# Performance work log

Hardware: AMD Instinct MI355X
Metric: run time of the kernel (lower is better)

The kernel has to match this reference:

```python
import jax, jax.numpy as jnp
import numpy as np

D_MODEL = 2048
D_STATE = 64
D_CONV = 4
EXPAND = 2
HEADDIM = 64
NGROUPS = 1
CHUNK = 64
D_INNER = EXPAND * D_MODEL            # 4096
NHEADS = D_INNER // HEADDIM           # 64
D_XBC = D_INNER + 2 * NGROUPS * D_STATE
D_IN_PROJ = 2 * D_INNER + 2 * NGROUPS * D_STATE + NHEADS


def setup_inputs():
    key = jax.random.key(0)
    ks = jax.random.split(key, 8)
    B, L = 2, 4096
    u = jax.random.normal(ks[0], (B, L, D_MODEL), jnp.float32)
    W_in = jax.random.normal(ks[1], (D_IN_PROJ, D_MODEL), jnp.float32) * 0.02
    conv_w = jax.random.normal(ks[2], (D_XBC, D_CONV), jnp.float32) * 0.2
    conv_b = jnp.zeros((D_XBC,), jnp.float32)
    dt = jnp.exp(jax.random.uniform(ks[3], (NHEADS,)) * (np.log(0.1) - np.log(0.001)) + np.log(0.001))
    dt = jnp.clip(dt, 1e-4)
    dt_bias = dt + jnp.log(-jnp.expm1(-dt))
    A_log = jnp.log(jax.random.uniform(ks[4], (NHEADS,), minval=1.0, maxval=16.0))
    D_param = jnp.ones((NHEADS,), jnp.float32)
    norm_w = jnp.ones((D_INNER,), jnp.float32)
    W_out = jax.random.normal(ks[5], (D_MODEL, D_INNER), jnp.float32) * 0.02
    return dict(u=u, W_in=W_in, conv_w=conv_w, conv_b=conv_b, dt_bias=dt_bias,
                A_log=A_log, D_param=D_param, norm_w=norm_w, W_out=W_out)


def segsum(x):
    # x: (..., T) -> (..., T, T) with entry [l,s] = sum_{s< i <= l} x[i], -inf above diag
    T = x.shape[-1]
    mask_strict = jnp.tril(jnp.ones((T, T), bool), k=-1)
    mask_incl = jnp.tril(jnp.ones((T, T), bool), k=0)
    xe = jnp.where(mask_strict, x[..., :, None], 0.0)  # element [l,s] = x[l] if l>s
    xseg = jnp.cumsum(xe, axis=-2)
    return jnp.where(mask_incl, xseg, -jnp.inf)


def ssd_scan(X, A, Bm, Cm, block_len=CHUNK):
    # X: (b,L,h,p), A: (b,L,h), Bm/Cm: (b,L,h,n)
    b, seqlen, h, p = X.shape
    n = Bm.shape[-1]
    pad_len = (block_len - seqlen % block_len) % block_len
    if pad_len > 0:
        X = jnp.pad(X, ((0, 0), (0, pad_len), (0, 0), (0, 0)))
        A = jnp.pad(A, ((0, 0), (0, pad_len), (0, 0)))
        Bm = jnp.pad(Bm, ((0, 0), (0, pad_len), (0, 0), (0, 0)))
        Cm = jnp.pad(Cm, ((0, 0), (0, pad_len), (0, 0), (0, 0)))
    L = X.shape[1]
    c = L // block_len
    Xc = X.reshape(b, c, block_len, h, p)
    Ac = A.reshape(b, c, block_len, h).transpose(0, 3, 1, 2)  # (b,h,c,l)
    Bc = Bm.reshape(b, c, block_len, h, n)
    Cc = Cm.reshape(b, c, block_len, h, n)
    A_cum = jnp.cumsum(Ac, axis=-1)                           # (b,h,c,l)
    Lmat = jnp.exp(segsum(Ac))                                # (b,h,c,l,s)
    CB = jnp.einsum('bclhn,bcshn->bhcls', Cc, Bc)
    Y_diag = jnp.einsum('bhcls,bcshp->bhclp', CB * Lmat, Xc)
    decay_states = jnp.exp(A_cum[..., -1:] - A_cum)           # (b,h,c,l)
    states = jnp.einsum('bhcl,bclhn,bclhp->bhcpn', decay_states, Bc, Xc)
    init = jnp.zeros((b, h, 1, p, n), X.dtype)
    states = jnp.concatenate([init, states], axis=2)          # (b,h,c+1,p,n)
    chunk_decay = jnp.pad(A_cum[..., -1], ((0, 0), (0, 0), (1, 0)))  # (b,h,c+1)
    decay_chunk = jnp.exp(segsum(chunk_decay))                # (b,h,c+1,c+1)
    new_states = jnp.einsum('bhzc,bhcpn->bhzpn', decay_chunk, states)[:, :, :-1]
    Y_off = jnp.einsum('bclhn,bhcpn,bhcl->bhclp', Cc, new_states, jnp.exp(A_cum))
    Y = (Y_diag + Y_off).transpose(0, 2, 3, 1, 4).reshape(b, L, h, p)
    if pad_len > 0:
        Y = Y[:, :seqlen]
    return Y


def rmsnorm_grouped(x, w, ngroups, eps=1e-5):
    gs = x.shape[-1] // ngroups
    xg = x.reshape(*x.shape[:-1], ngroups, gs)
    xg = xg * jax.lax.rsqrt(jnp.mean(xg * xg, axis=-1, keepdims=True) + eps)
    return xg.reshape(x.shape) * w


def reference(u, W_in, conv_w, conv_b, dt_bias, A_log, D_param, norm_w, W_out):
    B, L, _ = u.shape
    zxbcdt = u @ W_in.T                                      # (B,L,d_in_proj)
    z = zxbcdt[..., :D_INNER]
    xBC = zxbcdt[..., D_INNER:D_INNER + D_XBC]
    dt = zxbcdt[..., D_INNER + D_XBC:]
    # causal depthwise conv1d, kernel D_CONV, left-pad D_CONV-1
    xpad = jnp.pad(xBC, ((0, 0), (D_CONV - 1, 0), (0, 0)))
    conv = conv_b
    for k in range(D_CONV):
        conv = conv + conv_w[:, k] * xpad[:, k:k + L, :]
    xBC = jax.nn.silu(conv)
    x = xBC[..., :D_INNER].reshape(B, L, NHEADS, HEADDIM)
    B_ssm = xBC[..., D_INNER:D_INNER + NGROUPS * D_STATE].reshape(B, L, NGROUPS, D_STATE)
    C_ssm = xBC[..., D_INNER + NGROUPS * D_STATE:].reshape(B, L, NGROUPS, D_STATE)
    if NGROUPS < NHEADS:
        rep = NHEADS // NGROUPS
        B_ssm = jnp.repeat(B_ssm, rep, axis=2)
        C_ssm = jnp.repeat(C_ssm, rep, axis=2)
    dt = jax.nn.softplus(dt + dt_bias)                        # (B,L,nheads)
    A = -jnp.exp(A_log)                                       # (nheads,)
    y = ssd_scan(x * dt[..., None], A * dt, B_ssm, C_ssm, block_len=CHUNK)
    y = y + D_param[:, None] * x
    y = y.reshape(B, L, D_INNER)
    y = rmsnorm_grouped(y * jax.nn.silu(z), norm_w, NGROUPS)
    return y @ W_out.T
```

## Files before the change

kernel.cpp:

```cpp
#include <hip/hip_runtime.h>
#include <hip/hip_bf16.h>
#include <math.h>

#define SEQ       4096
#define DMODEL    2048
#define DINNER    4096
#define DXBC      4224
#define NPROJ     8384
#define NHEADS    64
#define HDIM      64
#define DSTATE    64
#define NCHUNK    64
#define XLD       4352

typedef __attribute__((ext_vector_type(8))) _Float16 half8;
typedef __attribute__((ext_vector_type(2))) _Float16 half2v;
typedef __attribute__((ext_vector_type(4))) float floatx4;

__device__ __forceinline__ void async_copy16(void* lds, const void* g) {
  __builtin_amdgcn_global_load_lds(
      (const __attribute__((address_space(1))) unsigned int*)g,
      (__attribute__((address_space(3))) unsigned int*)lds, 16, 0, 0);
}

__device__ __forceinline__ float silu_f(float x) { return x / (1.f + __expf(-x)); }

__device__ __forceinline__ void cvt8(const float* __restrict__ s, _Float16* __restrict__ d) {
  float4 a = *(const float4*)s;
  float4 b = *(const float4*)(s + 4);
  half8 h;
  h[0] = (_Float16)a.x; h[1] = (_Float16)a.y; h[2] = (_Float16)a.z; h[3] = (_Float16)a.w;
  h[4] = (_Float16)b.x; h[5] = (_Float16)b.y; h[6] = (_Float16)b.z; h[7] = (_Float16)b.w;
  *(half8*)d = h;
}

__global__ void diag_kernel(float* out, float v) { out[0] = v; }

#define U_N8 (SEQ * DMODEL / 8)
__global__ void cvt_in_kernel(const float* __restrict__ u, const float* __restrict__ W_in,
                              _Float16* __restrict__ ubf, _Float16* __restrict__ winbf) {
  int i = blockIdx.x * 256 + threadIdx.x;
  if (i < U_N8) {
    cvt8(u + (size_t)i * 8, ubf + (size_t)i * 8);
  } else {
    int j = i - U_N8;
    int row = j >> 8;
    size_t off = (size_t)j * 8;
    if (row < NPROJ) {
      cvt8(W_in + off, winbf + off);
    } else {
      half8 zz = {};
      *(half8*)(winbf + off) = zz;
    }
  }
}

__global__ void cvt8_kernel(const float* __restrict__ src, _Float16* __restrict__ dst, int n8) {
  int i = blockIdx.x * 256 + threadIdx.x;
  if (i < n8) cvt8(src + (size_t)i * 8, dst + (size_t)i * 8);
}

template <typename OT>
__global__ __launch_bounds__(256) void gemm_bt64(
    const _Float16* __restrict__ A, const _Float16* __restrict__ B,
    OT* __restrict__ C0, OT* __restrict__ C1, int K,
    int ldc0, int ldc1, int ncol0, int tiles_m, int tiles_n) {
  __shared__ __align__(16) _Float16 As[128 * 64];
  __shared__ __align__(16) _Float16 Bs[128 * 64];
  int t = threadIdx.x;
  int nt = tiles_m * tiles_n;
  int id = blockIdx.x;
  int id2 = ((nt & 7) == 0) ? ((id & 7) * (nt >> 3) + (id >> 3)) : id;
  int wband = tiles_m << 2;
  int g = id2 / wband;
  int rm = id2 - g * wband;
  int bw = tiles_n - (g << 2); if (bw > 4) bw = 4;
  int pn = (g << 2) + rm % bw;
  int pm = rm / bw;
  int m0 = pm * 128, n0 = pn * 128;

  int w = t >> 6, lane = t & 63, q = lane >> 4, r = lane & 15;
  int wm = (w >> 1) * 64, wn = (w & 1) * 64;
  int rowoff = lane >> 3;
  int chunkoff = ((lane & 7) ^ rowoff) * 8;
  const _Float16* gA[4];
  const _Float16* gB[4];
#pragma unroll
  for (int i = 0; i < 4; ++i) {
    gA[i] = A + (size_t)(m0 + i * 32 + w * 8 + rowoff) * K + chunkoff;
    gB[i] = B + (size_t)(n0 + i * 32 + w * 8 + rowoff) * K + chunkoff;
  }
  floatx4 acc[4][4] = {};
  for (int k0 = 0; k0 < K; k0 += 64) {
#pragma unroll
    for (int i = 0; i < 4; ++i) {
      async_copy16(As + (i * 32 + w * 8) * 64, gA[i] + k0);
      async_copy16(Bs + (i * 32 + w * 8) * 64, gB[i] + k0);
    }
    __syncthreads();
#pragma unroll
    for (int kk = 0; kk < 64; kk += 32) {
      half8 af[4], bf[4];
#pragma unroll
      for (int im = 0; im < 4; ++im) {
        int R = wm + im * 16 + r;
        af[im] = *(const half8*)&As[R * 64 + ((((kk >> 3) + q) ^ (R & 7)) << 3)];
      }
#pragma unroll
      for (int in = 0; in < 4; ++in) {
        int R = wn + in * 16 + r;
        bf[in] = *(const half8*)&Bs[R * 64 + ((((kk >> 3) + q) ^ (R & 7)) << 3)];
      }
#pragma unroll
      for (int im = 0; im < 4; ++im)
#pragma unroll
        for (int in = 0; in < 4; ++in)
          acc[im][in] =
              __builtin_amdgcn_mfma_f32_16x16x32_f16(af[im], bf[in], acc[im][in], 0, 0, 0);
    }
    __syncthreads();
  }
  OT* Cp = (n0 < ncol0) ? C0 : C1;
  int ldc = (n0 < ncol0) ? ldc0 : ldc1;
  int cb = (n0 < ncol0) ? n0 : n0 - ncol0;
#pragma unroll
  for (int im = 0; im < 4; ++im)
#pragma unroll
    for (int in = 0; in < 4; ++in)
#pragma unroll
      for (int i = 0; i < 4; ++i)
        Cp[(size_t)(m0 + wm + im * 16 + q * 4 + i) * ldc + cb + wn + in * 16 + r] =
            (OT)acc[im][in][i];
}

__global__ void conv_silu_kernel(const _Float16* __restrict__ xin, const float* __restrict__ conv_w,
                                 const float* __restrict__ conv_b, _Float16* __restrict__ xcv) {
  int idx = blockIdx.x * 256 + threadIdx.x;
  int l = idx / (DXBC / 2);
  int c = (idx - l * (DXBC / 2)) * 2;
  const _Float16* zc = xin + (size_t)l * XLD + c;
  float a0 = conv_b[c], a1 = conv_b[c + 1];
#pragma unroll
  for (int k = 0; k < 4; ++k) {
    int off = k - 3;
    if (l + off >= 0) {
      half2v v = *(const half2v*)(zc + (long)off * XLD);
      a0 += conv_w[c * 4 + k] * (float)v[0];
      a1 += conv_w[c * 4 + 4 + k] * (float)v[1];
    }
  }
  half2v o;
  o[0] = (_Float16)silu_f(a0);
  o[1] = (_Float16)silu_f(a1);
  *(half2v*)(xcv + (size_t)l * DXBC + c) = o;
}

__global__ __launch_bounds__(256) void dtscan_kernel(
    const _Float16* __restrict__ dtraw, const float* __restrict__ dt_bias,
    const float* __restrict__ A_log, float* __restrict__ dtp,
    float* __restrict__ acum, float* __restrict__ chs) {
  int c = blockIdx.x;
  __shared__ float dAs[64 * 65];
  int t = threadIdx.x;
  int h = t & 63;
  float bias = dt_bias[h];
  float negA = -__expf(A_log[h]);
#pragma unroll
  for (int i = 0; i < 16; ++i) {
    int l = i * 4 + (t >> 6);
    int row = c * 64 + l;
    float x = (float)dtraw[(size_t)row * XLD + h] + bias;
    float dtv = (x > 20.f) ? x : log1pf(__expf(x));
    dtp[(size_t)row * 64 + h] = dtv;
    dAs[l * 65 + h] = negA * dtv;
  }
  __syncthreads();
  if (t < 64) {
    float a = 0.f;
    size_t base = ((size_t)c * 64 + t) * 64;
    for (int l = 0; l < 64; ++l) {
      a += dAs[l * 65 + t];
      acum[base + l] = a;
    }
    chs[c * 64 + t] = a;
  }
}

__global__ __launch_bounds__(256) void states_kernel(
    const _Float16* __restrict__ xcv, const float* __restrict__ dtp,
    const float* __restrict__ acum, const float* __restrict__ chs,
    _Float16* __restrict__ states) {
  int bid = blockIdx.x;
  int c = bid & 63, h = bid >> 6;
  int row0 = c * 64;
  int acbase = (c * 64 + h) * 64;
  __shared__ __align__(16) _Float16 XdT[64 * 72];
  __shared__ __align__(16) _Float16 BdT[64 * 72];
  __shared__ float dec[64];
  int t = threadIdx.x;
  if (t < 64) dec[t] = __expf(chs[acbase >> 6] - acum[acbase + t]);
  __syncthreads();
#pragma unroll
  for (int i = 0; i < 16; ++i) {
    int flat = i * 256 + t;
    int l = flat >> 6, col = flat & 63;
    int grow = row0 + l;
    float dtv = dtp[(size_t)grow * 64 + h];
    float xv = (float)xcv[(size_t)grow * DXBC + h * 64 + col] * dtv;
    XdT[col * 72 + l] = (_Float16)xv;
    float bv = (float)xcv[(size_t)grow * DXBC + DINNER + col] * dec[l];
    BdT[col * 72 + l] = (_Float16)bv;
  }
  __syncthreads();
  int w = t >> 6, lane = t & 63, q = lane >> 4, r = lane & 15;
#pragma unroll
  for (int in = 0; in < 4; ++in) {
    floatx4 a4 = {0.f, 0.f, 0.f, 0.f};
#pragma unroll
    for (int k0 = 0; k0 < 64; k0 += 32) {
      half8 af = *(const half8*)&XdT[(w * 16 + r) * 72 + k0 + q * 8];
      half8 bf = *(const half8*)&BdT[(in * 16 + r) * 72 + k0 + q * 8];
      a4 = __builtin_amdgcn_mfma_f32_16x16x32_f16(af, bf, a4, 0, 0, 0);
    }
#pragma unroll
    for (int i = 0; i < 4; ++i)
      states[((size_t)bid * 64 + (w * 16 + q * 4 + i)) * 64 + in * 16 + r] = (_Float16)a4[i];
  }
}

__global__ __launch_bounds__(256) void scan_kernel(_Float16* __restrict__ states,
                                                   const float* __restrict__ chs) {
  int bid = blockIdx.x;
  int h = bid >> 4, seg = bid & 15;
  int e = seg * 256 + threadIdx.x;
  float carry = 0.f;
#pragma unroll 2
  for (int c = 0; c < 64; ++c) {
    size_t idx = ((size_t)(h * 64 + c)) * 4096 + e;
    float s = (float)states[idx];
    states[idx] = (_Float16)carry;
    carry = carry * __expf(chs[c * 64 + h]) + s;
  }
}

__global__ __launch_bounds__(256) void yout_kernel(
    const _Float16* __restrict__ xcv, const float* __restrict__ dtp,
    const float* __restrict__ acum, const _Float16* __restrict__ sin_,
    const float* __restrict__ Dp, _Float16* __restrict__ Y) {
  int bid = blockIdx.x;
  int c = bid & 63, h = bid >> 6;
  int row0 = c * 64;
  int acbase = (c * 64 + h) * 64;
  __shared__ __align__(16) _Float16 Cs[64 * 72];
  __shared__ __align__(16) _Float16 Bt[64 * 72];
  __shared__ __align__(16) _Float16 XdT[64 * 72];
  __shared__ __align__(16) _Float16 Ms[64 * 72];
  __shared__ float acs[64];
  int t = threadIdx.x;
  if (t < 64) acs[t] = acum[acbase + t];
#pragma unroll
  for (int i = 0; i < 16; ++i) {
    int flat = i * 256 + t;
    int l = flat >> 6, col = flat & 63;
    int grow = row0 + l;
    const _Float16* rp = xcv + (size_t)grow * DXBC;
    Cs[l * 72 + col] = rp[DINNER + DSTATE + col];
    Bt[l * 72 + col] = rp[DINNER + col];
    float xv = (float)rp[h * 64 + col] * dtp[(size_t)grow * 64 + h];
    XdT[col * 72 + l] = (_Float16)xv;
  }
  __syncthreads();
  int w = t >> 6, lane = t & 63, q = lane >> 4, r = lane & 15;
  int m = w * 16 + r;
#pragma unroll
  for (int in = 0; in < 4; ++in) {
    floatx4 cb = {0.f, 0.f, 0.f, 0.f};
#pragma unroll
    for (int k0 = 0; k0 < 64; k0 += 32) {
      half8 af = *(const half8*)&Cs[m * 72 + k0 + q * 8];
      half8 bf = *(const half8*)&Bt[(in * 16 + r) * 72 + k0 + q * 8];
      cb = __builtin_amdgcn_mfma_f32_16x16x32_f16(af, bf, cb, 0, 0, 0);
    }
#pragma unroll
    for (int i = 0; i < 4; ++i) {
      int l = w * 16 + q * 4 + i;
      int s = in * 16 + r;
      float v = (s <= l) ? cb[i] * __expf(acs[l] - acs[s]) : 0.f;
      Ms[l * 72 + s] = (_Float16)v;
    }
  }
  __syncthreads();
  size_t sbase = (size_t)bid * 4096;
  float Dh = Dp[h];
#pragma unroll
  for (int in = 0; in < 4; ++in) {
    floatx4 acc = {0.f, 0.f, 0.f, 0.f};
#pragma unroll
    for (int k0 = 0; k0 < 64; k0 += 32) {
      half8 af = *(const half8*)&Cs[m * 72 + k0 + q * 8];
      half8 bf = *(const half8*)&sin_[sbase + (size_t)(in * 16 + r) * 64 + k0 + q * 8];
      acc = __builtin_amdgcn_mfma_f32_16x16x32_f16(af, bf, acc, 0, 0, 0);
    }
#pragma unroll
    for (int i = 0; i < 4; ++i) acc[i] *= __expf(acs[w * 16 + q * 4 + i]);
#pragma unroll
    for (int k0 = 0; k0 < 64; k0 += 32) {
      half8 af = *(const half8*)&Ms[m * 72 + k0 + q * 8];
      half8 bf = *(const half8*)&XdT[(in * 16 + r) * 72 + k0 + q * 8];
      acc = __builtin_amdgcn_mfma_f32_16x16x32_f16(af, bf, acc, 0, 0, 0);
    }
#pragma unroll
    for (int i = 0; i < 4; ++i) {
      int l = w * 16 + q * 4 + i;
      int p = in * 16 + r;
      int grow = row0 + l;
      float xv = (float)xcv[(size_t)grow * DXBC + h * 64 + p];
      Y[(size_t)grow * DINNER + h * 64 + p] = (_Float16)(acc[i] + Dh * xv);
    }
  }
}

__global__ __launch_bounds__(256) void rmsnorm_kernel(const _Float16* __restrict__ Y,
                                                      _Float16* __restrict__ Z,
                                                      const float* __restrict__ norm_w) {
  int row = blockIdx.x;
  const half8* y8 = (const half8*)(Y + (size_t)row * DINNER);
  half8* z8 = (half8*)(Z + (size_t)row * DINNER);
  __shared__ float red[4];
  int t = threadIdx.x;
  float g[16];
  float ss = 0.f;
#pragma unroll
  for (int i = 0; i < 2; ++i) {
    int j = i * 256 + t;
    half8 yv = y8[j];
    half8 zv = z8[j];
#pragma unroll
    for (int e = 0; e < 8; ++e) {
      float gv = (float)yv[e] * silu_f((float)zv[e]);
      g[i * 8 + e] = gv;
      ss += gv * gv;
    }
  }
#pragma unroll
  for (int o = 32; o > 0; o >>= 1) ss += __shfl_down(ss, o, 64);
  if ((t & 63) == 0) red[t >> 6] = ss;
  __syncthreads();
  float rs = rsqrtf((red[0] + red[1] + red[2] + red[3]) / (float)DINNER + 1e-5f);
#pragma unroll
  for (int i = 0; i < 2; ++i) {
    int j = i * 256 + t;
    const float4* w4 = (const float4*)(norm_w + j * 8);
    float4 wa = w4[0], wb = w4[1];
    half8 o;
    o[0] = (_Float16)(g[i * 8 + 0] * rs * wa.x);
    o[1] = (_Float16)(g[i * 8 + 1] * rs * wa.y);
    o[2] = (_Float16)(g[i * 8 + 2] * rs * wa.z);
    o[3] = (_Float16)(g[i * 8 + 3] * rs * wa.w);
    o[4] = (_Float16)(g[i * 8 + 4] * rs * wb.x);
    o[5] = (_Float16)(g[i * 8 + 5] * rs * wb.y);
    o[6] = (_Float16)(g[i * 8 + 6] * rs * wb.z);
    o[7] = (_Float16)(g[i * 8 + 7] * rs * wb.w);
    z8[j] = o;
  }
}

extern "C" void kernel_launch(void* const* d_in, const int* in_sizes, int n_in,
                              void* d_out, int out_size, void* d_ws, size_t ws_size,
                              hipStream_t stream) {
  const float* u       = (const float*)d_in[0];
  const float* W_in    = (const float*)d_in[1];
  const float* conv_w  = (const float*)d_in[2];
  const float* conv_b  = (const float*)d_in[3];
  const float* dt_bias = (const float*)d_in[4];
  const float* A_log   = (const float*)d_in[5];
  const float* D_param = (const float*)d_in[6];
  const float* norm_w  = (const float*)d_in[7];
  const float* W_out   = (const float*)d_in[8];
  float* out = (float*)d_out;
  char* ws = (char*)d_ws;

  const size_t off_z      = 0;
  const size_t off_xbcdt  = 33554432ULL;
  const size_t off_Y      = 33554432ULL;
  const size_t off_xcv    = 69206016ULL;
  const size_t off_winbf  = 69206016ULL;
  const size_t off_states = 103809024ULL;
  const size_t off_ubf    = 103809024ULL;
  const size_t off_wout   = 103809024ULL;
  const size_t off_dtp    = 137363456ULL;
  const size_t off_acum   = 139460608ULL;
  const size_t off_chs    = 140509184ULL;
  const size_t ws_needed  = 140525568ULL;
  if (ws_size < ws_needed) {
    diag_kernel<<<1, 1, 0, stream>>>(out, (float)ws_size);
    return;
  }

  _Float16* zb     = (_Float16*)(ws + off_z);
  _Float16* xbcdtb = (_Float16*)(ws + off_xbcdt);
  _Float16* Yb     = (_Float16*)(ws + off_Y);
  _Float16* xcv    = (_Float16*)(ws + off_xcv);
  _Float16* winbf  = (_Float16*)(ws + off_winbf);
  _Float16* states = (_Float16*)(ws + off_states);
  _Float16* ubf    = (_Float16*)(ws + off_ubf);
  _Float16* woutbf = (_Float16*)(ws + off_wout);
  float*    dtp    = (float*)(ws + off_dtp);
  float*    acum   = (float*)(ws + off_acum);
  float*    chs    = (float*)(ws + off_chs);

  for (int b = 0; b < 2; ++b) {
    const float* ub = u + (size_t)b * SEQ * DMODEL;
    float* outb = out + (size_t)b * SEQ * DMODEL;

    cvt_in_kernel<<<U_N8 / 256 + 8448, 256, 0, stream>>>(ub, W_in, ubf, winbf);

    gemm_bt64<_Float16><<<32 * 66, 256, 0, stream>>>(
        ubf, winbf, zb, xbcdtb, DMODEL, DINNER, XLD, DINNER, 32, 66);

    conv_silu_kernel<<<SEQ * (DXBC / 2) / 256, 256, 0, stream>>>(xbcdtb, conv_w, conv_b, xcv);
    dtscan_kernel<<<NCHUNK, 256, 0, stream>>>(xbcdtb + DXBC, dt_bias, A_log, dtp, acum, chs);

    states_kernel<<<NHEADS * NCHUNK, 256, 0, stream>>>(xcv, dtp, acum, chs, states);
    scan_kernel<<<NHEADS * 16, 256, 0, stream>>>(states, chs);
    yout_kernel<<<NHEADS * NCHUNK, 256, 0, stream>>>(xcv, dtp, acum, states, D_param, Yb);

    rmsnorm_kernel<<<SEQ, 256, 0, stream>>>(Yb, zb, norm_w);

    cvt8_kernel<<<(DMODEL * DINNER / 8 + 255) / 256, 256, 0, stream>>>(
        W_out, woutbf, DMODEL * DINNER / 8);
    gemm_bt64<float><<<32 * 16, 256, 0, stream>>>(
        zb, woutbf, outb, outb, DINNER, DMODEL, DMODEL, 1 << 30, 32, 16);
  }
}
```

Baseline: 1.163 ms.

## Convert weights once per call when workspace allows; fuse conv and dt-scan launches

When the workspace is large enough, the code gets a new buffer layout. W_in and W_out are then converted to fp16 once before the batch loop instead of once per batch, and each batch converts only u. The conv+SiLU and dt softplus/cumsum kernels become one launch, with block ranges picking the role. The inter-chunk scan now prefetches the next state load to hide latency. The cost is a second workspace layout that must be kept consistent with the small-workspace fallback.

Result: faster. 1.133 ms (-2.6%).

```diff
diff --git a/kernel.cpp b/kernel.cpp
--- a/kernel.cpp
+++ b/kernel.cpp
@@ -35,6 +35,23 @@
 }
 
 __global__ void diag_kernel(float* out, float v) { out[0] = v; }
+
+__global__ void cvt8_kernel(const float* __restrict__ src, _Float16* __restrict__ dst, int n8) {
+  int i = blockIdx.x * 256 + threadIdx.x;
+  if (i < n8) cvt8(src + (size_t)i * 8, dst + (size_t)i * 8);
+}
+
+__global__ void cvt_win_kernel(const float* __restrict__ W_in, _Float16* __restrict__ dst) {
+  int i = blockIdx.x * 256 + threadIdx.x;
+  int row = i >> 8;
+  size_t off = (size_t)i * 8;
+  if (row < NPROJ) {
+    cvt8(W_in + off, dst + off);
+  } else {
+    half8 zz = {};
+    *(half8*)(dst + off) = zz;
+  }
+}
 
 #define U_N8 (SEQ * DMODEL / 8)
 __global__ void cvt_in_kernel(const float* __restrict__ u, const float* __restrict__ W_in,
@@ -53,11 +70,6 @@
       *(half8*)(winbf + off) = zz;
     }
   }
-}
-
-__global__ void cvt8_kernel(const float* __restrict__ src, _Float16* __restrict__ dst, int n8) {
-  int i = blockIdx.x * 256 + threadIdx.x;
-  if (i < n8) cvt8(src + (size_t)i * 8, dst + (size_t)i * 8);
 }
 
 template <typename OT>
@@ -133,56 +145,58 @@
             (OT)acc[im][in][i];
 }
 
-__global__ void conv_silu_kernel(const _Float16* __restrict__ xin, const float* __restrict__ conv_w,
-                                 const float* __restrict__ conv_b, _Float16* __restrict__ xcv) {
-  int idx = blockIdx.x * 256 + threadIdx.x;
-  int l = idx / (DXBC / 2);
-  int c = (idx - l * (DXBC / 2)) * 2;
-  const _Float16* zc = xin + (size_t)l * XLD + c;
-  float a0 = conv_b[c], a1 = conv_b[c + 1];
-#pragma unroll
-  for (int k = 0; k < 4; ++k) {
-    int off = k - 3;
-    if (l + off >= 0) {
-      half2v v = *(const half2v*)(zc + (long)off * XLD);
-      a0 += conv_w[c * 4 + k] * (float)v[0];
-      a1 += conv_w[c * 4 + 4 + k] * (float)v[1];
-    }
-  }
-  half2v o;
-  o[0] = (_Float16)silu_f(a0);
-  o[1] = (_Float16)silu_f(a1);
-  *(half2v*)(xcv + (size_t)l * DXBC + c) = o;
-}
-
-__global__ __launch_bounds__(256) void dtscan_kernel(
-    const _Float16* __restrict__ dtraw, const float* __restrict__ dt_bias,
-    const float* __restrict__ A_log, float* __restrict__ dtp,
-    float* __restrict__ acum, float* __restrict__ chs) {
-  int c = blockIdx.x;
-  __shared__ float dAs[64 * 65];
+#define CONVB (SEQ * (DXBC / 2) / 256)
+__global__ __launch_bounds__(256) void conv_dtscan_kernel(
+    const _Float16* __restrict__ xin, const float* __restrict__ conv_w,
+    const float* __restrict__ conv_b, _Float16* __restrict__ xcv,
+    const float* __restrict__ dt_bias, const float* __restrict__ A_log,
+    float* __restrict__ dtp, float* __restrict__ acum, float* __restrict__ chs) {
   int t = threadIdx.x;
-  int h = t & 63;
-  float bias = dt_bias[h];
-  float negA = -__expf(A_log[h]);
-#pragma unroll
-  for (int i = 0; i < 16; ++i) {
-    int l = i * 4 + (t >> 6);
-    int row = c * 64 + l;
-    float x = (float)dtraw[(size_t)row * XLD + h] + bias;
-    float dtv = (x > 20.f) ? x : log1pf(__expf(x));
-    dtp[(size_t)row * 64 + h] = dtv;
-    dAs[l * 65 + h] = negA * dtv;
-  }
-  __syncthreads();
-  if (t < 64) {
-    float a = 0.f;
-    size_t base = ((size_t)c * 64 + t) * 64;
-    for (int l = 0; l < 64; ++l) {
-      a += dAs[l * 65 + t];
-      acum[base + l] = a;
-    }
-    chs[c * 64 + t] = a;
+  if (blockIdx.x < CONVB) {
+    int idx = blockIdx.x * 256 + t;
+    int l = idx / (DXBC / 2);
+    int c = (idx - l * (DXBC / 2)) * 2;
+    const _Float16* zc = xin + (size_t)l * XLD + c;
+    float a0 = conv_b[c], a1 = conv_b[c + 1];
+#pragma unroll
+    for (int k = 0; k < 4; ++k) {
+      int off = k - 3;
+      if (l + off >= 0) {
+        half2v v = *(const half2v*)(zc + (long)off * XLD);
+        a0 += conv_w[c * 4 + k] * (float)v[0];
+        a1 += conv_w[c * 4 + 4 + k] * (float)v[1];
+      }
+    }
+    half2v o;
+    o[0] = (_Float16)silu_f(a0);
+    o[1] = (_Float16)silu_f(a1);
+    *(half2v*)(xcv + (size_t)l * DXBC + c) = o;
+  } else {
+    __shared__ float dAs[64 * 65];
+    int c = blockIdx.x - CONVB;
+    int h = t & 63;
+    const _Float16* dtraw = xin + DXBC;
+    float bias = dt_bias[h];
+    float negA = -__expf(A_log[h]);
+#pragma unroll
+    for (int i = 0; i < 16; ++i) {
+      int l = i * 4 + (t >> 6);
+      int row = c * 64 + l;
+      float x = (float)dtraw[(size_t)row * XLD + h] + bias;
+      float dtv = (x > 20.f) ? x : log1pf(__expf(x));
+      dtp[(size_t)row * 64 + h] = dtv;
+      dAs[l * 65 + h] = negA * dtv;
+    }
+    __syncthreads();
+    if (t < 64) {
+      float a = 0.f;
+      size_t base = ((size_t)c * 64 + t) * 64;
+      for (int l = 0; l < 64; ++l) {
+        a += dAs[l * 65 + t];
+        acum[base + l] = a;
+      }
+      chs[c * 64 + t] = a;
+    }
   }
 }
 
@@ -232,14 +246,16 @@
                                                    const float* __restrict__ chs) {
   int bid = blockIdx.x;
   int h = bid >> 4, seg = bid & 15;
-  int e = seg * 256 + threadIdx.x;
+  size_t base = ((size_t)h * 64) * 4096 + seg * 256 + threadIdx.x;
   float carry = 0.f;
-#pragma unroll 2
+  float s_cur = (float)states[base];
   for (int c = 0; c < 64; ++c) {
-    size_t idx = ((size_t)(h * 64 + c)) * 4096 + e;
-    float s = (float)states[idx];
+    size_t idx = base + (size_t)c * 4096;
+    float s_next = (c < 63) ? (float)states[idx + 4096] : 0.f;
+    float ec = __expf(chs[c * 64 + h]);
     states[idx] = (_Float16)carry;
-    carry = carry * __expf(chs[c * 64 + h]) + s;
+    carry = carry * ec + s_cur;
+    s_cur = s_next;
   }
 }
 
@@ -380,46 +396,63 @@
   float* out = (float*)d_out;
   char* ws = (char*)d_ws;
 
-  const size_t off_z      = 0;
-  const size_t off_xbcdt  = 33554432ULL;
-  const size_t off_Y      = 33554432ULL;
-  const size_t off_xcv    = 69206016ULL;
-  const size_t off_winbf  = 69206016ULL;
-  const size_t off_states = 103809024ULL;
-  const size_t off_ubf    = 103809024ULL;
-  const size_t off_wout   = 103809024ULL;
-  const size_t off_dtp    = 137363456ULL;
-  const size_t off_acum   = 139460608ULL;
-  const size_t off_chs    = 140509184ULL;
-  const size_t ws_needed  = 140525568ULL;
-  if (ws_size < ws_needed) {
+  const size_t NEED_MID   = 192954368ULL;
+  const size_t NEED_SMALL = 140525568ULL;
+  bool big = (ws_size >= NEED_MID);
+  if (!big && ws_size < NEED_SMALL) {
     diag_kernel<<<1, 1, 0, stream>>>(out, (float)ws_size);
     return;
   }
 
-  _Float16* zb     = (_Float16*)(ws + off_z);
-  _Float16* xbcdtb = (_Float16*)(ws + off_xbcdt);
-  _Float16* Yb     = (_Float16*)(ws + off_Y);
-  _Float16* xcv    = (_Float16*)(ws + off_xcv);
-  _Float16* winbf  = (_Float16*)(ws + off_winbf);
-  _Float16* states = (_Float16*)(ws + off_states);
-  _Float16* ubf    = (_Float16*)(ws + off_ubf);
-  _Float16* woutbf = (_Float16*)(ws + off_wout);
-  float*    dtp    = (float*)(ws + off_dtp);
-  float*    acum   = (float*)(ws + off_acum);
-  float*    chs    = (float*)(ws + off_chs);
+  _Float16 *winbf, *woutbf, *zb, *xbcdtb, *Yb, *xcv, *states, *ubf;
+  float *dtp, *acum, *chs;
+  if (big) {
+    winbf  = (_Float16*)(ws + 0);
+    woutbf = (_Float16*)(ws + 34603008ULL);
+    zb     = (_Float16*)(ws + 51380224ULL);
+    xbcdtb = (_Float16*)(ws + 84934656ULL);
+    Yb     = xbcdtb;
+    xcv    = (_Float16*)(ws + 120586240ULL);
+    states = (_Float16*)(ws + 155189248ULL);
+    ubf    = states;
+    dtp    = (float*)(ws + 188743680ULL);
+    acum   = (float*)(ws + 190840832ULL);
+    chs    = (float*)(ws + 192937984ULL);
+  } else {
+    zb     = (_Float16*)(ws + 0);
+    xbcdtb = (_Float16*)(ws + 33554432ULL);
+    Yb     = xbcdtb;
+    xcv    = (_Float16*)(ws + 69206016ULL);
+    winbf  = xcv;
+    states = (_Float16*)(ws + 103809024ULL);
+    ubf    = states;
+    woutbf = states;
+    dtp    = (float*)(ws + 137363456ULL);
+    acum   = (float*)(ws + 139460608ULL);
+    chs    = (float*)(ws + 140509184ULL);
+  }
+
+  if (big) {
+    cvt_win_kernel<<<8448, 256, 0, stream>>>(W_in, winbf);
+    cvt8_kernel<<<DMODEL * DINNER / 8 / 256, 256, 0, stream>>>(
+        W_out, woutbf, DMODEL * DINNER / 8);
+  }
 
   for (int b = 0; b < 2; ++b) {
     const float* ub = u + (size_t)b * SEQ * DMODEL;
     float* outb = out + (size_t)b * SEQ * DMODEL;
 
-    cvt_in_kernel<<<U_N8 / 256 + 8448, 256, 0, stream>>>(ub, W_in, ubf, winbf);
+    if (big) {
+      cvt8_kernel<<<U_N8 / 256, 256, 0, stream>>>(ub, ubf, U_N8);
+    } else {
+      cvt_in_kernel<<<U_N8 / 256 + 8448, 256, 0, stream>>>(ub, W_in, ubf, winbf);
+    }
 
     gemm_bt64<_Float16><<<32 * 66, 256, 0, stream>>>(
         ubf, winbf, zb, xbcdtb, DMODEL, DINNER, XLD, DINNER, 32, 66);
 
-    conv_silu_kernel<<<SEQ * (DXBC / 2) / 256, 256, 0, stream>>>(xbcdtb, conv_w, conv_b, xcv);
-    dtscan_kernel<<<NCHUNK, 256, 0, stream>>>(xbcdtb + DXBC, dt_bias, A_log, dtp, acum, chs);
+    conv_dtscan_kernel<<<CONVB + NCHUNK, 256, 0, stream>>>(
+        xbcdtb, conv_w, conv_b, xcv, dt_bias, A_log, dtp, acum, chs);
 
     states_kernel<<<NHEADS * NCHUNK, 256, 0, stream>>>(xcv, dtp, acum, chs, states);
     scan_kernel<<<NHEADS * 16, 256, 0, stream>>>(states, chs);
@@ -427,8 +460,10 @@
 
     rmsnorm_kernel<<<SEQ, 256, 0, stream>>>(Yb, zb, norm_w);
 
-    cvt8_kernel<<<(DMODEL * DINNER / 8 + 255) / 256, 256, 0, stream>>>(
-        W_out, woutbf, DMODEL * DINNER / 8);
+    if (!big) {
+      cvt8_kernel<<<DMODEL * DINNER / 8 / 256, 256, 0, stream>>>(
+          W_out, woutbf, DMODEL * DINNER / 8);
+    }
     gemm_bt64<float><<<32 * 16, 256, 0, stream>>>(
         zb, woutbf, outb, outb, DINNER, DMODEL, DMODEL, 1 << 30, 32, 16);
   }
```
